# Performance work log

Measured on AMD Instinct MI355X. Metric: run time of the kernel, lower is better.

Reference implementation:

```python
import jax, jax.numpy as jnp
import numpy as np

B, M, F, U = 2048, 64, 512, 512  # batch, number_masks, num_features, units=ceil(F**1.0)

def setup_inputs() -> dict:
    key = jax.random.key(0)
    kx, kw = jax.random.split(key)
    x = jax.random.normal(kx, (B, M, F), dtype=jnp.float32)
    # glorot-uniform style init like keras Dense default
    limit = np.sqrt(6.0 / (F + U)).astype(np.float32)
    W = jax.random.uniform(kw, (M, F, U), dtype=jnp.float32, minval=-limit, maxval=limit)
    b = jnp.zeros((M, U), dtype=jnp.float32)
    return {"x": x, "W": W, "b": b}

def reference(x, W, b):
    # Per-mask Dense applied in a Python loop in the original == one batched GEMM.
    # y[b,m,u] = relu(sum_f x[b,m,f] * W[m,f,u] + b[m,u])
    y = jax.nn.relu(jnp.einsum('bmf,mfu->bmu', x, W) + b[None, :, :])
    # Concatenate along feature axis -> [B, M*U]
    return y.reshape(y.shape[0], -1)
```

## Files before the change

kernel.cpp:

```cpp
#include <hip/hip_runtime.h>
#include <hip/hip_bf16.h>


typedef __attribute__((ext_vector_type(8))) short bf16x8;
typedef __attribute__((ext_vector_type(4))) float f32x4;

#define LDS_S 40

__device__ __forceinline__ unsigned pk_bf16(float a, float b) {
    float2 t; t.x = a; t.y = b;
    __hip_bfloat162 h = __float22bfloat162_rn(t);
    union { __hip_bfloat162 h; unsigned u; } cv;
    cv.h = h;
    return cv.u;
}

__global__ void pdense_kernel(const float* __restrict__ X,
                              const float* __restrict__ Wp,
                              const float* __restrict__ bias,
                              float* __restrict__ Out) {
    __shared__ short ldsA[128 * LDS_S];
    __shared__ short ldsB[128 * LDS_S];

    const int tid  = threadIdx.x;
    const int lane = tid & 63;
    const int wave = tid >> 6;
    const int q    = lane >> 4;
    const int ln   = lane & 15;
    const int wr   = (wave >> 1) * 64;
    const int wc   = (wave & 1) * 64;

    const int m    = blockIdx.y;
    const int bt   = blockIdx.x & 15;
    const int ut   = blockIdx.x >> 4;
    const int row0 = bt * 128;
    const int col0 = ut * 128;

    const int ar0 = tid >> 2;
    const int ak0 = (tid & 3) * 8;
    const int ar1 = ar0 + 64;
    const float* aP0 = X + (size_t)(row0 + ar0) * 32768 + m * 512 + ak0;
    const float* aP1 = X + (size_t)(row0 + ar1) * 32768 + m * 512 + ak0;

    const int k0 = (tid & 7) * 4;
    const int u0 = (tid >> 3) * 4;
    const float* bP = Wp + (size_t)m * 262144 + (size_t)k0 * 512 + col0 + u0;

    f32x4 acc[4][4];
    #pragma unroll
    for (int i = 0; i < 4; ++i)
        #pragma unroll
        for (int j = 0; j < 4; ++j)
            acc[i][j] = (f32x4)0.0f;

    float4 a_pre[2][2];
    float4 b_pre[4];

    a_pre[0][0] = ((const float4*)aP0)[0];
    a_pre[0][1] = ((const float4*)aP0)[1];
    a_pre[1][0] = ((const float4*)aP1)[0];
    a_pre[1][1] = ((const float4*)aP1)[1];
    #pragma unroll
    for (int i = 0; i < 4; ++i)
        b_pre[i] = *(const float4*)(bP + (size_t)i * 512);

    for (int kt = 0; kt < 16; ++kt) {
        {
            uint4 w0, w1;
            w0.x = pk_bf16(a_pre[0][0].x, a_pre[0][0].y);
            w0.y = pk_bf16(a_pre[0][0].z, a_pre[0][0].w);
            w0.z = pk_bf16(a_pre[0][1].x, a_pre[0][1].y);
            w0.w = pk_bf16(a_pre[0][1].z, a_pre[0][1].w);
            *(uint4*)&ldsA[ar0 * LDS_S + ak0] = w0;
            w1.x = pk_bf16(a_pre[1][0].x, a_pre[1][0].y);
            w1.y = pk_bf16(a_pre[1][0].z, a_pre[1][0].w);
            w1.z = pk_bf16(a_pre[1][1].x, a_pre[1][1].y);
            w1.w = pk_bf16(a_pre[1][1].z, a_pre[1][1].w);
            *(uint4*)&ldsA[ar1 * LDS_S + ak0] = w1;
            #pragma unroll
            for (int j = 0; j < 4; ++j) {
                float c0 = ((const float*)&b_pre[0])[j];
                float c1 = ((const float*)&b_pre[1])[j];
                float c2 = ((const float*)&b_pre[2])[j];
                float c3 = ((const float*)&b_pre[3])[j];
                uint2 wv;
                wv.x = pk_bf16(c0, c1);
                wv.y = pk_bf16(c2, c3);
                *(uint2*)&ldsB[(u0 + j) * LDS_S + k0] = wv;
            }
        }
        __syncthreads();

        if (kt + 1 < 16) {
            const int ko = (kt + 1) * 32;
            a_pre[0][0] = ((const float4*)(aP0 + ko))[0];
            a_pre[0][1] = ((const float4*)(aP0 + ko))[1];
            a_pre[1][0] = ((const float4*)(aP1 + ko))[0];
            a_pre[1][1] = ((const float4*)(aP1 + ko))[1];
            #pragma unroll
            for (int i = 0; i < 4; ++i)
                b_pre[i] = *(const float4*)(bP + (size_t)(ko + i) * 512);
        }

        bf16x8 aF[4], bF[4];
        #pragma unroll
        for (int i = 0; i < 4; ++i)
            aF[i] = *(const bf16x8*)&ldsA[(wr + i * 16 + ln) * LDS_S + q * 8];
        #pragma unroll
        for (int j = 0; j < 4; ++j)
            bF[j] = *(const bf16x8*)&ldsB[(wc + j * 16 + ln) * LDS_S + q * 8];
        #pragma unroll
        for (int i = 0; i < 4; ++i)
            #pragma unroll
            for (int j = 0; j < 4; ++j)
                acc[i][j] = __builtin_amdgcn_mfma_f32_16x16x32_bf16(aF[i], bF[j], acc[i][j], 0, 0, 0);

        __syncthreads();
    }

    #pragma unroll
    for (int j = 0; j < 4; ++j) {
        const int c = col0 + wc + j * 16 + ln;
        const float bv = bias[m * 512 + c];
        #pragma unroll
        for (int i = 0; i < 4; ++i) {
            const int r = row0 + wr + i * 16 + q * 4;
            float* op = Out + (size_t)r * 32768 + m * 512 + c;
            f32x4 v = acc[i][j];
            #pragma unroll
            for (int t = 0; t < 4; ++t) {
                float val = v[t] + bv;
                op[(size_t)t * 32768] = val > 0.0f ? val : 0.0f;
            }
        }
    }
}

extern "C" void kernel_launch(void* const* d_in, const int* in_sizes, int n_in,
                              void* d_out, int out_size, void* d_ws, size_t ws_size,
                              hipStream_t stream) {
    const float* x    = (const float*)d_in[0];
    const float* W    = (const float*)d_in[1];
    const float* bias = (const float*)d_in[2];
    float* out = (float*)d_out;
    dim3 grid(64, 64);
    dim3 block(256);
    hipLaunchKernelGGL(pdense_kernel, grid, block, 0, stream, x, W, bias, out);
}
```

Baseline: 617.1 us.

## Pre-transpose W to bf16 workspace and double-buffer LDS in GEMM

A prep kernel transposes W into a bf16 [m][u][f] workspace, so the main kernel loads B tiles as contiguous 16-byte bf16 vectors with no per-iteration conversion or scatter. The main kernel double-buffers the LDS tiles, using one barrier per k-step and writing the next tile after the MFMAs. Block ordering changes so that the four column tiles sharing an X row block sit next to each other, which should improve X reuse in cache. This adds an extra kernel launch and a 32 MB workspace write and read, and keeps the old kernel as a fallback when the workspace is too small.

Measured after the change: 612.3 us. Within noise of the previous version (-0.8%).

```diff
diff --git a/kernel.cpp b/kernel.cpp
--- a/kernel.cpp
+++ b/kernel.cpp
@@ -15,10 +15,155 @@
     return cv.u;
 }
 
-__global__ void pdense_kernel(const float* __restrict__ X,
-                              const float* __restrict__ Wp,
-                              const float* __restrict__ bias,
-                              float* __restrict__ Out) {
+__global__ void wt_prep_kernel(const float* __restrict__ W, short* __restrict__ Wt) {
+    __shared__ float t[32][33];
+    const int m  = blockIdx.z;
+    const int f0 = blockIdx.y * 32;
+    const int u0 = blockIdx.x * 32;
+    const int tx = threadIdx.x;
+    const int ty = threadIdx.y;
+    const float* src = W + ((size_t)m * 512 + f0) * 512 + u0;
+    #pragma unroll
+    for (int i = 0; i < 4; ++i)
+        t[ty + 8 * i][tx] = src[(size_t)(ty + 8 * i) * 512 + tx];
+    __syncthreads();
+    short* dst = Wt + ((size_t)m * 512 + u0) * 512 + f0;
+    #pragma unroll
+    for (int i = 0; i < 4; ++i) {
+        float v = t[tx][ty + 8 * i];
+        dst[(size_t)(ty + 8 * i) * 512 + tx] = (short)(pk_bf16(v, v) & 0xffff);
+    }
+}
+
+__global__ __launch_bounds__(256) void pdense_main(const float* __restrict__ X,
+                                                   const short* __restrict__ Wt,
+                                                   const float* __restrict__ bias,
+                                                   float* __restrict__ Out) {
+    __shared__ short ldsA[2][128 * LDS_S];
+    __shared__ short ldsB[2][128 * LDS_S];
+
+    const int tid  = threadIdx.x;
+    const int lane = tid & 63;
+    const int wave = tid >> 6;
+    const int q    = lane >> 4;
+    const int ln   = lane & 15;
+    const int wr   = (wave >> 1) * 64;
+    const int wc   = (wave & 1) * 64;
+
+    const int m    = blockIdx.y;
+    const int ut   = blockIdx.x & 3;
+    const int bt   = blockIdx.x >> 2;
+    const int row0 = bt * 128;
+    const int col0 = ut * 128;
+
+    const int r0  = tid >> 2;
+    const int k8  = (tid & 3) * 8;
+    const int r1  = r0 + 64;
+    const float* aP0 = X + (size_t)(row0 + r0) * 32768 + m * 512 + k8;
+    const float* aP1 = X + (size_t)(row0 + r1) * 32768 + m * 512 + k8;
+    const short* bP0 = Wt + (size_t)m * 262144 + (size_t)(col0 + r0) * 512 + k8;
+    const short* bP1 = bP0 + 64 * 512;
+
+    f32x4 acc[4][4];
+    #pragma unroll
+    for (int i = 0; i < 4; ++i)
+        #pragma unroll
+        for (int j = 0; j < 4; ++j)
+            acc[i][j] = (f32x4)0.0f;
+
+    float4 a_pre[4];
+    uint4  b_pre[2];
+
+    a_pre[0] = ((const float4*)aP0)[0];
+    a_pre[1] = ((const float4*)aP0)[1];
+    a_pre[2] = ((const float4*)aP1)[0];
+    a_pre[3] = ((const float4*)aP1)[1];
+    b_pre[0] = *(const uint4*)bP0;
+    b_pre[1] = *(const uint4*)bP1;
+
+    {
+        uint4 w0, w1;
+        w0.x = pk_bf16(a_pre[0].x, a_pre[0].y);
+        w0.y = pk_bf16(a_pre[0].z, a_pre[0].w);
+        w0.z = pk_bf16(a_pre[1].x, a_pre[1].y);
+        w0.w = pk_bf16(a_pre[1].z, a_pre[1].w);
+        *(uint4*)&ldsA[0][r0 * LDS_S + k8] = w0;
+        w1.x = pk_bf16(a_pre[2].x, a_pre[2].y);
+        w1.y = pk_bf16(a_pre[2].z, a_pre[2].w);
+        w1.z = pk_bf16(a_pre[3].x, a_pre[3].y);
+        w1.w = pk_bf16(a_pre[3].z, a_pre[3].w);
+        *(uint4*)&ldsA[0][r1 * LDS_S + k8] = w1;
+        *(uint4*)&ldsB[0][r0 * LDS_S + k8] = b_pre[0];
+        *(uint4*)&ldsB[0][r1 * LDS_S + k8] = b_pre[1];
+    }
+
+    for (int kt = 0; kt < 16; ++kt) {
+        const int p = kt & 1;
+        __syncthreads();
+
+        if (kt + 1 < 16) {
+            const int ko = (kt + 1) * 32;
+            a_pre[0] = ((const float4*)(aP0 + ko))[0];
+            a_pre[1] = ((const float4*)(aP0 + ko))[1];
+            a_pre[2] = ((const float4*)(aP1 + ko))[0];
+            a_pre[3] = ((const float4*)(aP1 + ko))[1];
+            b_pre[0] = *(const uint4*)(bP0 + ko);
+            b_pre[1] = *(const uint4*)(bP1 + ko);
+        }
+
+        bf16x8 aF[4], bF[4];
+        #pragma unroll
+        for (int i = 0; i < 4; ++i)
+            aF[i] = *(const bf16x8*)&ldsA[p][(wr + i * 16 + ln) * LDS_S + q * 8];
+        #pragma unroll
+        for (int j = 0; j < 4; ++j)
+            bF[j] = *(const bf16x8*)&ldsB[p][(wc + j * 16 + ln) * LDS_S + q * 8];
+        #pragma unroll
+        for (int i = 0; i < 4; ++i)
+            #pragma unroll
+            for (int j = 0; j < 4; ++j)
+                acc[i][j] = __builtin_amdgcn_mfma_f32_16x16x32_bf16(aF[i], bF[j], acc[i][j], 0, 0, 0);
+
+        if (kt + 1 < 16) {
+            const int pn = p ^ 1;
+            uint4 w0, w1;
+            w0.x = pk_bf16(a_pre[0].x, a_pre[0].y);
+            w0.y = pk_bf16(a_pre[0].z, a_pre[0].w);
+            w0.z = pk_bf16(a_pre[1].x, a_pre[1].y);
+            w0.w = pk_bf16(a_pre[1].z, a_pre[1].w);
+            *(uint4*)&ldsA[pn][r0 * LDS_S + k8] = w0;
+            w1.x = pk_bf16(a_pre[2].x, a_pre[2].y);
+            w1.y = pk_bf16(a_pre[2].z, a_pre[2].w);
+            w1.z = pk_bf16(a_pre[3].x, a_pre[3].y);
+            w1.w = pk_bf16(a_pre[3].z, a_pre[3].w);
+            *(uint4*)&ldsA[pn][r1 * LDS_S + k8] = w1;
+            *(uint4*)&ldsB[pn][r0 * LDS_S + k8] = b_pre[0];
+            *(uint4*)&ldsB[pn][r1 * LDS_S + k8] = b_pre[1];
+        }
+    }
+
+    #pragma unroll
+    for (int j = 0; j < 4; ++j) {
+        const int c = col0 + wc + j * 16 + ln;
+        const float bv = bias[m * 512 + c];
+        #pragma unroll
+        for (int i = 0; i < 4; ++i) {
+            const int r = row0 + wr + i * 16 + q * 4;
+            float* op = Out + (size_t)r * 32768 + m * 512 + c;
+            f32x4 v = acc[i][j];
+            #pragma unroll
+            for (int t = 0; t < 4; ++t) {
+                float val = v[t] + bv;
+                op[(size_t)t * 32768] = val > 0.0f ? val : 0.0f;
+            }
+        }
+    }
+}
+
+__global__ void pdense_fallback(const float* __restrict__ X,
+                                const float* __restrict__ Wp,
+                                const float* __restrict__ bias,
+                                float* __restrict__ Out) {
     __shared__ short ldsA[128 * LDS_S];
     __shared__ short ldsB[128 * LDS_S];
 
@@ -143,7 +288,13 @@
     const float* W    = (const float*)d_in[1];
     const float* bias = (const float*)d_in[2];
     float* out = (float*)d_out;
-    dim3 grid(64, 64);
-    dim3 block(256);
-    hipLaunchKernelGGL(pdense_kernel, grid, block, 0, stream, x, W, bias, out);
-}
+
+    const size_t wt_bytes = (size_t)64 * 512 * 512 * sizeof(short);
+    if (ws_size >= wt_bytes) {
+        short* Wt = (short*)d_ws;
+        hipLaunchKernelGGL(wt_prep_kernel, dim3(16, 16, 64), dim3(32, 8), 0, stream, W, Wt);
+        hipLaunchKernelGGL(pdense_main, dim3(64, 64), dim3(256), 0, stream, x, Wt, bias, out);
+    } else {
+        hipLaunchKernelGGL(pdense_fallback, dim3(64, 64), dim3(256), 0, stream, W ? x : x, W, bias, out);
+    }
+}
```
